# Performance work log

Measured on AMD Instinct MI355X. Metric: run time of the kernel, lower is better.

Reference implementation:

```python
import jax, jax.numpy as jnp
import numpy as np


def _grid_edges(H, W, diag):
    # Freudenthal triangulation edges: horizontal, vertical, and one diagonal per cell.
    idx = np.arange(H * W, dtype=np.int64).reshape(H, W)
    us = [idx[:, :-1].ravel(), idx[:-1, :].ravel()]
    vs = [idx[:, 1:].ravel(), idx[1:, :].ravel()]
    if diag == "main":
        us.append(idx[:-1, :-1].ravel()); vs.append(idx[1:, 1:].ravel())
    else:  # anti-diagonal = dual connectivity of the main-diagonal triangulation
        us.append(idx[1:, :-1].ravel()); vs.append(idx[:-1, 1:].ravel())
    return np.concatenate(us), np.concatenate(vs)


def _find(parent, x):
    r = x
    while parent[r] != r:
        r = parent[r]
    while parent[x] != r:  # path compression
        parent[x], x = r, parent[x]
    return r


def _sublevel_h0_pairs(g, u, v, boundary_idx=None):
    # 0-dim persistence of the sublevel (lower-star) filtration of vertex values g
    # over edge list (u, v); returns (birth_vertex, death_vertex) index pairs for all
    # FINITE bars (elder rule).  If boundary_idx is given, a virtual node at -inf is
    # attached to those vertices (models the unbounded outside region; never dies).
    n = g.shape[0]
    if boundary_idx is not None:
        u = np.concatenate([u, boundary_idx])
        v = np.concatenate([v, np.full(boundary_idx.shape[0], n, dtype=np.int64)])
        g = np.concatenate([g, np.array([-np.inf])])
    wu, wv = g[u], g[v]
    widx = np.where(wu >= wv, u, v)  # vertex whose value is the edge entry time
    order = np.argsort(np.maximum(wu, wv), kind="stable")
    parent = np.arange(g.shape[0], dtype=np.int64)
    birth = np.arange(g.shape[0], dtype=np.int64)  # component-min vertex per root
    pb, pd = [], []
    for ei in order:
        ra, rb = _find(parent, u[ei]), _find(parent, v[ei])
        if ra == rb:
            continue
        if g[birth[ra]] <= g[birth[rb]]:
            old, young = ra, rb
        else:
            old, young = rb, ra
        pb.append(birth[young]); pd.append(widx[ei])  # younger component dies here
        parent[young] = old
    return np.asarray(pb, dtype=np.int64), np.asarray(pd, dtype=np.int64)


def _toploss_pairs(f2d):
    # Critical-vertex pairs whose value differences make up the TopLoss value.
    H, W = f2d.shape
    f = f2d.ravel().astype(np.float64)
    # --- dim-0 superlevel persistence: sublevel union-find on -f ---
    u0, v0 = _grid_edges(H, W, "main")
    b0, d0 = _sublevel_h0_pairs(-f, u0, v0)  # b0: component argmax of f, d0: merge vertex
    # --- dim-1 superlevel persistence via Alexander duality:  H1({f>=t}) bars ---
    # correspond to H0 bars of the sublevel filtration of f on the dual connectivity,
    # with a virtual outside component attached to the image boundary.
    u1, v1 = _grid_edges(H, W, "anti")
    idx = np.arange(H * W, dtype=np.int64).reshape(H, W)
    boundary = np.unique(np.concatenate([idx[0], idx[-1], idx[:, 0], idx[:, -1]]))
    m_idx, M_idx = _sublevel_h0_pairs(f, u1, v1, boundary)
    # H1 bar = (birth f[M], death f[m]); PartialSumBarcodeLengths(dim=1, skip=1)
    # drops the single longest bar.
    L = f[M_idx] - f[m_idx]
    keep = np.argsort(-L, kind="stable")[1:]
    return b0, d0, M_idx[keep], m_idx[keep]


def setup_inputs() -> dict:
    key = jax.random.key(0)
    beta = jax.random.uniform(key, (256, 256), dtype=jnp.float32)
    return {"beta": beta}


def reference(beta):
    # pairing indices are a (piecewise-constant) function of the data; computed on host
    b0, d0, b1, d1 = _toploss_pairs(np.asarray(beta))
    fb = beta.ravel()
    # SumBarcodeLengths(dim=0): sum of finite H0 bar lengths (birth - death, superlevel)
    # + PartialSumBarcodeLengths(dim=1, skip=1): sum of all-but-longest H1 bar lengths
    return (fb[b0].sum() - fb[d0].sum()) + (fb[b1].sum() - fb[d1].sum())
```

## Files before the change

### kernel.cpp

```cpp
#include <hip/hip_runtime.h>

typedef unsigned int u32;
typedef unsigned short u16;
typedef unsigned long long u64;

#define NV 65536
#define TS 32
#define TVERTS 1024
#define TILES 64
#define SMAX 8192
#define VIRTID 8191
#define EMAX 65536


__global__ __launch_bounds__(1024) void k_tile(const float* __restrict__ f,
    u32* compD, u64* meD, float* maxD, double* partialT, u32* hdr, double* sumsG) {
  const int inst = blockIdx.z;
  const int bx = blockIdx.x;
  const int R0 = (bx >> 3) * TS, C0 = (bx & 7) * TS;
  const int tid = threadIdx.x;
  const int l = tid;
  const int lr = l >> 5, lc = l & 31;
  const int gr = R0 + lr, gc = C0 + lc;
  const int gv = gr * 256 + gc;

  __shared__ float sf[TVERTS];
  __shared__ u16 parL[TVERTS];
  __shared__ u64 meL[TVERTS];
  __shared__ u32 s_rank;
  __shared__ double s_red[16];
  __shared__ float s_redf[16];

  if (inst == 0 && bx == 0 && tid == 0) {
    hdr[0] = 0u; hdr[1] = 0u; hdr[2] = 0u; sumsG[0] = 0.0; sumsG[1] = 0.0;
  }
  if (tid < 128) meD[(size_t)inst * SMAX + (size_t)bx * 128 + tid] = ~0ull;
  if (tid == 0) s_rank = 0u;

  float x = f[gv];
  sf[l] = x; parL[l] = (u16)l;
  float fm = x;
  for (int o = 32; o > 0; o >>= 1) fm = fmaxf(fm, __shfl_down(fm, o));
  if ((tid & 63) == 0) s_redf[tid >> 6] = fm;
  __syncthreads();
  if (inst == 0 && tid == 0) {
    float m = s_redf[0];
    #pragma unroll
    for (int i = 1; i < 16; ++i) m = fmaxf(m, s_redf[i]);
    maxD[bx] = m;
  }

  auto amin = [](u64* slot, u64 p) {
    if (p < *slot) atomicMin(slot, p);
  };

  double wsum = 0.0;
  for (int round = 0; round < 14; ++round) {
    if (round > 0) {
      u32 xx = parL[l];
      for (int g = 0; g < TVERTS; ++g) { u32 p = parL[xx]; if (p == xx) break; xx = p; }
      parL[l] = (u16)xx;
      __syncthreads();
    }
    meL[l] = ~0ull;
    __syncthreads();
    {
      float fv = sf[l];
      u32 rv = parL[l];
      auto mk = [&](float w, int code) -> u64 {
        u32 kb = __float_as_uint(w); if (!inst) kb = ~kb;
        return ((u64)kb << 13) | (u64)(u32)(l << 3) | (u64)code;
      };
      auto pushI = [&](int nl, int code) {
        u32 rn = parL[nl];
        if (rn == rv) return;
        float w = inst ? fmaxf(fv, sf[nl]) : fminf(fv, sf[nl]);
        u64 p = mk(w, code);
        amin(&meL[rv], p); amin(&meL[rn], p);
      };
      auto pushO = [&](float fu, int code) {
        float w = inst ? fmaxf(fv, fu) : fminf(fv, fu);
        amin(&meL[rv], mk(w, code));
      };
      if (gc < 255) { if (lc < TS - 1) pushI(l + 1, 0); else pushO(f[gv + 1], 0); }
      if (gc > 0 && lc == 0) pushO(f[gv - 1], 4);
      if (gr < 255) { if (lr < TS - 1) pushI(l + TS, 1); else pushO(f[gv + 256], 1); }
      if (gr > 0 && lr == 0) pushO(f[gv - 256], 5);
      if (inst == 0) {
        if (gr < 255 && gc < 255) { if (lr < TS - 1 && lc < TS - 1) pushI(l + TS + 1, 2); else pushO(f[gv + 257], 2); }
        if (gr > 0 && gc > 0 && (lr == 0 || lc == 0)) pushO(f[gv - 257], 6);
      } else {
        if (gr > 0 && gc < 255) { if (lr > 0 && lc < TS - 1) pushI(l - TS + 1, 2); else pushO(f[gv - 255], 2); }
        if (gr < 255 && gc > 0 && (lr == TS - 1 || lc == 0)) pushO(f[gv + 255], 6);
        if (gr == 0 || gr == 255 || gc == 0 || gc == 255) {
          u32 kb = __float_as_uint(sf[l]);
          amin(&meL[rv], ((u64)kb << 13) | (u64)(u32)(l << 3) | 3ull);
        }
      }
    }
    __syncthreads();
    u32 dec = ~0u;
    bool did = false;
    if (parL[l] == (u16)l) {
      u64 m = meL[l];
      if (m != ~0ull) {
        int code = (int)(m & 7);
        if (code < 3) {
          int vL = (int)((m >> 3) & 0x3FF);
          int vlr = vL >> 5, vlc = vL & 31;
          int nl = -1;
          if (code == 0) { if (vlc < TS - 1) nl = vL + 1; }
          else if (code == 1) { if (vlr < TS - 1) nl = vL + TS; }
          else {
            if (inst == 0) { if (vlr < TS - 1 && vlc < TS - 1) nl = vL + TS + 1; }
            else           { if (vlr > 0 && vlc < TS - 1)      nl = vL - TS + 1; }
          }
          if (nl >= 0) {
            u32 r1 = parL[vL], r2 = parL[nl];
            u32 n = (r1 == (u32)l) ? r2 : r1;
            u64 mn = meL[n];
            if (!(mn == m && (u32)l < n)) {
              dec = n;
              u32 kb = (u32)(m >> 13); if (!inst) kb = ~kb;
              wsum += (double)__uint_as_float(kb);
              did = true;
            }
          }
        }
      }
    }
    int cnt = __syncthreads_count(did ? 1 : 0);
    if (dec != ~0u) parL[l] = (u16)dec;
    __syncthreads();
    if (cnt == 0) break;
  }
  if (parL[l] == (u16)l) meL[l] = (u64)atomicAdd(&s_rank, 1u);
  __syncthreads();
  {
    u32 xx = parL[l];
    for (int g = 0; g < TVERTS; ++g) { u32 p = parL[xx]; if (p == xx) break; xx = p; }
    compD[(size_t)inst * NV + gv] = (u32)(bx * 128) + (u32)meL[xx];
  }
  double wt = wsum;
  for (int o = 32; o > 0; o >>= 1) wt += __shfl_down(wt, o);
  if ((tid & 63) == 0) s_red[tid >> 6] = wt;
  __syncthreads();
  if (tid == 0) {
    double t = 0.0;
    #pragma unroll
    for (int i = 0; i < 16; ++i) t += s_red[i];
    partialT[inst * 64 + bx] = t;
  }
}

__global__ __launch_bounds__(256) void k_emit(const float* __restrict__ f,
    const u32* __restrict__ compD, u32* hdr, u64* eb, u64* meD) {
  const int inst = blockIdx.z;
  const u32* __restrict__ cd = compD + (size_t)inst * NV;
  u64* eo = eb + (size_t)inst * 2 * EMAX;
  u64* me = meD + (size_t)inst * SMAX;
  const int tid = threadIdx.x;
  const int lane = tid & 63;
  int v = blockIdx.x * 256 + tid;
  int gr = v >> 8, gc = v & 255;
  float fv = f[v];
  u32 c0 = cd[v];

  __shared__ u64 s_ed[1024];
  __shared__ u32 s_cnt, s_base;
  if (tid == 0) s_cnt = 0u;
  __syncthreads();

  auto emit = [&](bool has, u32 key, u32 c1) {
    u64 pack = 0;
    if (has) {
      pack = ((u64)key << 26) | ((u64)c0 << 13) | (u64)c1;
      if (pack < me[c0]) atomicMin(&me[c0], pack);
      if (pack < me[c1]) atomicMin(&me[c1], pack);
    }
    u64 mask = __ballot(has);
    if (mask == 0) return;
    int lead = __ffsll((long long)mask) - 1;
    u32 base = 0;
    if (lane == lead) base = atomicAdd(&s_cnt, (u32)__popcll(mask));
    base = __shfl(base, lead);
    if (has) s_ed[base + (u32)__popcll(mask & ((1ull << lane) - 1ull))] = pack;
  };
  { bool has = false; u32 key = 0, c1 = 0;
    if (gc < 255) { c1 = cd[v + 1]; if (c1 != c0) { float w = inst ? fmaxf(fv, f[v + 1]) : fminf(fv, f[v + 1]); key = __float_as_uint(w); if (!inst) key = ~key; has = true; } }
    emit(has, key, c1); }
  { bool has = false; u32 key = 0, c1 = 0;
    if (gr < 255) { c1 = cd[v + 256]; if (c1 != c0) { float w = inst ? fmaxf(fv, f[v + 256]) : fminf(fv, f[v + 256]); key = __float_as_uint(w); if (!inst) key = ~key; has = true; } }
    emit(has, key, c1); }
  { bool has = false; u32 key = 0, c1 = 0;
    if (inst == 0) { if (gr < 255 && gc < 255) { c1 = cd[v + 257]; if (c1 != c0) { key = ~__float_as_uint(fminf(fv, f[v + 257])); has = true; } } }
    else { if (gr > 0 && gc < 255) { c1 = cd[v - 255]; if (c1 != c0) { key = __float_as_uint(fmaxf(fv, f[v - 255])); has = true; } } }
    emit(has, key, c1); }
  { bool has = false; u32 key = 0;
    if (inst == 1 && (gr == 0 || gr == 255 || gc == 0 || gc == 255)) { key = __float_as_uint(fv); has = true; }
    emit(has, key, (u32)VIRTID); }

  __syncthreads();
  if (tid == 0) s_base = s_cnt ? atomicAdd(&hdr[inst], s_cnt) : 0u;
  __syncthreads();
  u32 n = s_cnt, base = s_base;
  for (u32 i = tid; i < n; i += 256) {
    u32 idx = base + i;
    if (idx < EMAX) eo[idx] = s_ed[i];
  }
}

__global__ __launch_bounds__(1024) void k_bor(const u32* __restrict__ hdr_ro,
    u64* eb, const u64* __restrict__ meD, const double* __restrict__ partialT,
    const float* __restrict__ maxD, double* sumsG, u32* done, float* out) {
  const int inst = blockIdx.z;
  const int tid = threadIdx.x;
  const int lane = tid & 63;
  u32 E = hdr_ro[inst]; if (E > EMAX) E = EMAX;
  u64* cur = eb + (size_t)inst * 2 * EMAX;
  u64* nxt = cur + EMAX;

  __shared__ u16 parL[SMAX];
  __shared__ u64 meL[SMAX];
  __shared__ u16 actL[SMAX];
  __shared__ u32 s_cnt, s_act;
  __shared__ double s_red[16];
  __shared__ float s_mv;

  if (tid == 0) s_act = 0u;
  for (u32 s = tid; s < SMAX; s += 1024) parL[s] = (u16)s;
  __syncthreads();
  for (u32 s = tid; s < SMAX; s += 1024) {
    u64 m = meD[(size_t)inst * SMAX + s];
    meL[s] = m;
    bool act = (m != ~0ull);
    u64 mask = __ballot(act);
    if (mask) {
      int lead = __ffsll((long long)mask) - 1;
      u32 b = 0;
      if (lane == lead) b = atomicAdd(&s_act, (u32)__popcll(mask));
      b = __shfl(b, lead);
      if (act) actL[b + (u32)__popcll(mask & ((1ull << lane) - 1ull))] = (u16)s;
    }
  }
  __syncthreads();
  u32 A = s_act;
  double wsum = 0.0;

  for (int round = 0; round < 32 && A > 0 && E > 0; ++round) {
    for (u32 a = tid; a < A; a += 1024) {
      u32 s = actL[a]; u64 m = meL[s];
      u32 lo = (u32)(m >> 13) & 0x1FFFu, hi = (u32)m & 0x1FFFu;
      u32 n = (lo == s) ? hi : lo;
      u64 mn = meL[n];
      if (mn == m && s < n) continue;
      parL[s] = (u16)n;
      u32 kb = (u32)(m >> 26); if (!inst) kb = ~kb;
      wsum += (double)__uint_as_float(kb);
    }
    if (tid == 0) { s_cnt = 0u; s_act = 0u; }
    __syncthreads();
    for (u32 a = tid; a < A; a += 1024) {
      u32 s = actL[a];
      u32 x = parL[s];
      for (int g = 0; g < SMAX; ++g) { u32 p = parL[x]; if (p == x) break; x = p; }
      parL[s] = (u16)x;
      meL[s] = ~0ull;
    }
    __syncthreads();
    u32 Epad = (E + 1023u) & ~1023u;
    for (u32 e = tid; e < Epad; e += 1024) {
      bool alive = false; u64 np = 0; u32 rl = 0, rh = 0;
      if (e < E) {
        u64 w = cur[e];
        u32 lo = (u32)(w >> 13) & 0x1FFFu, hi = (u32)w & 0x1FFFu;
        rl = parL[lo]; rh = parL[hi];
        if (rl != rh) { alive = true; np = (w & ~(u64)0x3FFFFFFull) | ((u64)rl << 13) | (u64)rh; }
      }
      u64 mask = __ballot(alive);
      if (mask) {
        int lead = __ffsll((long long)mask) - 1;
        u32 base = 0;
        if (lane == lead) base = atomicAdd(&s_cnt, (u32)__popcll(mask));
        base = __shfl(base, lead);
        if (alive) {
          u32 ni = base + (u32)__popcll(mask & ((1ull << lane) - 1ull));
          nxt[ni] = np;
          if (np < meL[rl]) { u64 old = atomicMin(&meL[rl], np);
            if (old == ~0ull) { u32 a = atomicAdd(&s_act, 1u); actL[a] = (u16)rl; } }
          if (np < meL[rh]) { u64 old = atomicMin(&meL[rh], np);
            if (old == ~0ull) { u32 a = atomicAdd(&s_act, 1u); actL[a] = (u16)rh; } }
        }
      }
    }
    __syncthreads();
    E = s_cnt; A = s_act;
    u64* t = cur; cur = nxt; nxt = t;
  }

  double wt = wsum;
  for (int o = 32; o > 0; o >>= 1) wt += __shfl_down(wt, o);
  if (lane == 0) s_red[tid >> 6] = wt;
  __syncthreads();
  if (tid < 64) {
    float m = maxD[tid];
    for (int o = 32; o > 0; o >>= 1) m = fmaxf(m, __shfl_down(m, o));
    if (tid == 0) s_mv = m;
  }
  double v = 0.0;
  if (tid < 64) {
    v = partialT[inst * 64 + tid];
    if (tid < 16) v += s_red[tid];
    for (int o = 32; o > 0; o >>= 1) v += __shfl_down(v, o);
  }
  __syncthreads();
  if (tid == 0) {
    double total = v;
    atomicExch((u64*)&sumsG[inst], (u64)__double_as_longlong(total));
    __threadfence();
    u32 d = atomicAdd(done, 1u);
    if (d == 1u) {
      __threadfence();
      u64 ob = atomicAdd((u64*)&sumsG[1 - inst], 0ull);
      double other = __longlong_as_double((long long)ob);
      double w0 = (inst == 0) ? total : other;
      double w1 = (inst == 1) ? total : other;
      out[0] = (float)(w1 - w0 - (double)s_mv);
    }
  }
}

extern "C" void kernel_launch(void* const* d_in, const int* in_sizes, int n_in,
                              void* d_out, int out_size, void* d_ws, size_t ws_size,
                              hipStream_t stream) {
  const float* f = (const float*)d_in[0];
  float* out = (float*)d_out;
  char* ws = (char*)d_ws;
  double* sumsG    = (double*)ws;
  u32* hdr         = (u32*)(ws + 16);
  float* maxD      = (float*)(ws + 64);
  double* partialT = (double*)(ws + 512);
  u32* compD       = (u32*)(ws + 2048);
  u64* eb          = (u64*)(ws + 526336);
  u64* meD         = (u64*)(ws + 2623488);

  k_tile<<<dim3(TILES, 1, 2), dim3(1024), 0, stream>>>(f, compD, meD, maxD,
                                                       partialT, hdr, sumsG);
  k_emit<<<dim3(256, 1, 2), dim3(256), 0, stream>>>(f, compD, hdr, eb, meD);
  k_bor<<<dim3(1, 1, 2), dim3(1024), 0, stream>>>(hdr, eb, meD, partialT, maxD,
                                                  sumsG, hdr + 2, out);
}
```

Baseline: 107.2 us.

## Split first Boruvka round across 32 helper blocks feeding the single-block loop

```diff
diff --git a/kernel.cpp b/kernel.cpp
--- a/kernel.cpp
+++ b/kernel.cpp
@@ -11,10 +11,12 @@
 #define SMAX 8192
 #define VIRTID 8191
 #define EMAX 65536
+#define NW 32
 
 
 __global__ __launch_bounds__(1024) void k_tile(const float* __restrict__ f,
-    u32* compD, u64* meD, float* maxD, double* partialT, u32* hdr, double* sumsG) {
+    u32* compD, u64* meD, u64* meD2, float* maxD, double* partialT, u32* hdr,
+    double* sumsG) {
   const int inst = blockIdx.z;
   const int bx = blockIdx.x;
   const int R0 = (bx >> 3) * TS, C0 = (bx & 7) * TS;
@@ -32,9 +34,13 @@
   __shared__ float s_redf[16];
 
   if (inst == 0 && bx == 0 && tid == 0) {
-    hdr[0] = 0u; hdr[1] = 0u; hdr[2] = 0u; sumsG[0] = 0.0; sumsG[1] = 0.0;
-  }
-  if (tid < 128) meD[(size_t)inst * SMAX + (size_t)bx * 128 + tid] = ~0ull;
+    hdr[0] = 0u; hdr[1] = 0u; hdr[2] = 0u; hdr[3] = 0u; hdr[4] = 0u;
+    hdr[5] = 0u; hdr[6] = 0u; sumsG[0] = 0.0; sumsG[1] = 0.0;
+  }
+  if (tid < 128) {
+    meD [(size_t)inst * SMAX + (size_t)bx * 128 + tid] = ~0ull;
+    meD2[(size_t)inst * SMAX + (size_t)bx * 128 + tid] = ~0ull;
+  }
   if (tid == 0) s_rank = 0u;
 
   float x = f[gv];
@@ -211,27 +217,119 @@
 }
 
 __global__ __launch_bounds__(1024) void k_bor(const u32* __restrict__ hdr_ro,
-    u64* eb, const u64* __restrict__ meD, const double* __restrict__ partialT,
+    u32* hdr, u64* eb, const u64* __restrict__ meD, u64* meD2,
+    const double* __restrict__ partialT, u64* partialM,
     const float* __restrict__ maxD, double* sumsG, u32* done, float* out) {
   const int inst = blockIdx.z;
+  const int bx = blockIdx.x;
   const int tid = threadIdx.x;
   const int lane = tid & 63;
-  u32 E = hdr_ro[inst]; if (E > EMAX) E = EMAX;
-  u64* cur = eb + (size_t)inst * 2 * EMAX;
-  u64* nxt = cur + EMAX;
-
-  __shared__ u16 parL[SMAX];
-  __shared__ u64 meL[SMAX];
+  u64* e0 = eb + (size_t)inst * 2 * EMAX;
+  u64* e1 = e0 + EMAX;
+
+  __shared__ u64 shME[SMAX];
+  __shared__ u16 shPAR[SMAX];
   __shared__ u16 actL[SMAX];
-  __shared__ u32 s_cnt, s_act;
+  __shared__ u64 s_ed[1024];
+  __shared__ u32 s_cnt, s_act, s_base;
   __shared__ double s_red[16];
   __shared__ float s_mv;
 
-  if (tid == 0) s_act = 0u;
+  if (bx > 0) {
+    const u64* me62 = meD + (size_t)inst * SMAX;
+    u64* me61 = meD2 + (size_t)inst * SMAX;
+    for (u32 s = tid; s < SMAX; s += 1024) shME[s] = me62[s];
+    __syncthreads();
+    double wsum = 0.0;
+    for (u32 s = tid; s < SMAX; s += 1024) {
+      u16 p = (u16)s;
+      u64 m = shME[s];
+      if (m != ~0ull) {
+        u32 lo = (u32)(m >> 13) & 0x1FFFu, hi = (u32)m & 0x1FFFu;
+        u32 n = (lo == s) ? hi : lo;
+        if (!(shME[n] == m && s < n)) {
+          p = (u16)n;
+          if (bx == 1) {
+            u32 kb = (u32)(m >> 26); if (!inst) kb = ~kb;
+            wsum += (double)__uint_as_float(kb);
+          }
+        }
+      }
+      shPAR[s] = p;
+    }
+    __syncthreads();
+    for (u32 s = tid; s < SMAX; s += 1024) {
+      u32 x = shPAR[s];
+      if (shPAR[x] != (u16)x) {
+        for (int g = 0; g < SMAX; ++g) { u32 q = shPAR[x]; if (q == x) break; x = q; }
+        shPAR[s] = (u16)x;
+      }
+    }
+    __syncthreads();
+    {
+      double wt = wsum;
+      for (int o = 32; o > 0; o >>= 1) wt += __shfl_down(wt, o);
+      if (lane == 0) s_red[tid >> 6] = wt;
+      __syncthreads();
+      if (bx == 1 && tid == 0) {
+        double t = 0.0;
+        #pragma unroll
+        for (int i = 0; i < 16; ++i) t += s_red[i];
+        atomicExch(&partialM[inst], (u64)__double_as_longlong(t));
+      }
+    }
+    u32 E0v = hdr_ro[inst]; if (E0v > EMAX) E0v = EMAX;
+    for (u32 b0 = (u32)(bx - 1) * 1024u; b0 < E0v; b0 += (u32)NW * 1024u) {
+      if (tid == 0) s_cnt = 0u;
+      __syncthreads();
+      u32 e = b0 + (u32)tid;
+      bool alive = false; u64 np = 0;
+      if (e < E0v) {
+        u64 w = e0[e];
+        u32 rl = shPAR[(u32)(w >> 13) & 0x1FFFu];
+        u32 rh = shPAR[(u32)w & 0x1FFFu];
+        if (rl != rh) {
+          np = (w & ~(u64)0x3FFFFFFull) | ((u64)rl << 13) | (u64)rh;
+          alive = true;
+          if (np < me61[rl]) atomicMin(&me61[rl], np);
+          if (np < me61[rh]) atomicMin(&me61[rh], np);
+        }
+      }
+      u64 mask = __ballot(alive);
+      if (mask) {
+        int lead = __ffsll((long long)mask) - 1;
+        u32 base = 0;
+        if (lane == lead) base = atomicAdd(&s_cnt, (u32)__popcll(mask));
+        base = __shfl(base, lead);
+        if (alive) s_ed[base + (u32)__popcll(mask & ((1ull << lane) - 1ull))] = np;
+      }
+      __syncthreads();
+      if (tid == 0) s_base = s_cnt ? atomicAdd(&hdr[3 + inst], s_cnt) : 0u;
+      __syncthreads();
+      u32 n = s_cnt, bb = s_base;
+      for (u32 i = tid; i < n; i += 1024) {
+        u32 idx = bb + i;
+        if (idx < EMAX) atomicExch(&e1[idx], s_ed[i]);
+      }
+      __syncthreads();
+    }
+    __threadfence();
+    if (tid == 0) atomicAdd(&hdr[5 + inst], 1u);
+    return;
+  }
+
+  u16* parL = shPAR;
+  u64* meL = shME;
   for (u32 s = tid; s < SMAX; s += 1024) parL[s] = (u16)s;
-  __syncthreads();
+  if (tid == 0) {
+    s_act = 0u;
+    while (atomicAdd(&hdr[5 + inst], 0u) < (u32)NW) __builtin_amdgcn_s_sleep(10);
+  }
+  __syncthreads();
+  __threadfence();
+  u32 E = atomicAdd(&hdr[3 + inst], 0u); if (E > EMAX) E = EMAX;
   for (u32 s = tid; s < SMAX; s += 1024) {
-    u64 m = meD[(size_t)inst * SMAX + s];
+    u64 m = atomicAdd(&meD2[(size_t)inst * SMAX + s], 0ull);
     meL[s] = m;
     bool act = (m != ~0ull);
     u64 mask = __ballot(act);
@@ -246,6 +344,8 @@
   __syncthreads();
   u32 A = s_act;
   double wsum = 0.0;
+  u64* cur = e1;
+  u64* nxt = e0;
 
   for (int round = 0; round < 32 && A > 0 && E > 0; ++round) {
     for (u32 a = tid; a < A; a += 1024) {
@@ -315,7 +415,8 @@
   }
   __syncthreads();
   if (tid == 0) {
-    double total = v;
+    double w62 = __longlong_as_double((long long)atomicAdd(&partialM[inst], 0ull));
+    double total = v + w62;
     atomicExch((u64*)&sumsG[inst], (u64)__double_as_longlong(total));
     __threadfence();
     u32 d = atomicAdd(done, 1u);
@@ -339,14 +440,17 @@
   double* sumsG    = (double*)ws;
   u32* hdr         = (u32*)(ws + 16);
   float* maxD      = (float*)(ws + 64);
+  u64* partialM    = (u64*)(ws + 384);
   double* partialT = (double*)(ws + 512);
   u32* compD       = (u32*)(ws + 2048);
   u64* eb          = (u64*)(ws + 526336);
   u64* meD         = (u64*)(ws + 2623488);
-
-  k_tile<<<dim3(TILES, 1, 2), dim3(1024), 0, stream>>>(f, compD, meD, maxD,
+  u64* meD2        = (u64*)(ws + 2754560);
+
+  k_tile<<<dim3(TILES, 1, 2), dim3(1024), 0, stream>>>(f, compD, meD, meD2, maxD,
                                                        partialT, hdr, sumsG);
   k_emit<<<dim3(256, 1, 2), dim3(256), 0, stream>>>(f, compD, hdr, eb, meD);
-  k_bor<<<dim3(1, 1, 2), dim3(1024), 0, stream>>>(hdr, eb, meD, partialT, maxD,
-                                                  sumsG, hdr + 2, out);
+  k_bor<<<dim3(NW + 1, 1, 2), dim3(1024), 0, stream>>>(hdr, hdr, eb, meD, meD2,
+                                                       partialT, partialM, maxD,
+                                                       sumsG, hdr + 2, out);
 }
```

New measurement: 151.5 us. +41.3%, slower.
